# Kernel optimization log

Hardware: AMD Instinct MI355X
Metric: run time of the kernel (lower is better)

The kernel has to match this reference:

```python
import jax, jax.numpy as jnp
import numpy as np

B = 8388608
BASE_STABLE = 0.95
BASE_CHANGE = 0.05
TASK_WEIGHT = 1.0
EPS = 1e-8


def setup_inputs() -> dict:
    key = jax.random.key(0)
    k1, k2 = jax.random.split(key)
    logits = jax.random.normal(k1, (B, 2), dtype=jnp.float32)
    labels = jax.random.randint(k2, (B,), 0, 2, dtype=jnp.int64)
    return {"logits": logits, "labels": labels}


def reference(logits, labels):
    # softmax over class dim (C=2)
    p = jax.nn.softmax(logits, axis=1)
    p0 = p[:, 0]  # prob of 'stable' class
    p1 = p[:, 1]  # prob of 'change' class

    # Per-sample weights. In the original torch code these are computed via
    # .item() (python floats), i.e. they are constants w.r.t. autodiff.
    adj0 = jnp.maximum(0.0, p0 - BASE_STABLE) / (1.0 - BASE_STABLE)
    w0 = jnp.maximum(0.1, 1.0 - adj0 * 0.5)
    adj1 = jnp.maximum(0.0, p1 - BASE_CHANGE) / (1.0 - BASE_CHANGE)
    w1 = jnp.maximum(0.5, 2.0 - adj1)
    w0 = jax.lax.stop_gradient(w0)
    w1 = jax.lax.stop_gradient(w1)

    stable = labels == 0
    loss = jnp.where(stable,
                     -w0 * jnp.log(p0 + EPS),
                     -w1 * jnp.log(p1 + EPS))
    task_loss = loss.mean()
    total_loss = TASK_WEIGHT * task_loss
    return total_loss
```

## Files before the change

### kernel.cpp

```cpp
#include <hip/hip_runtime.h>


#define B_TOTAL   8388608
#define INV_B     (1.0f / 8388608.0f)
#define EPS_LOSS  1e-8f

#define NBLOCK    2048
#define NTHREAD   256
#define NTOT      (NBLOCK * NTHREAD)
#define NITER     (B_TOTAL / 2 / NTOT)

typedef float f4 __attribute__((ext_vector_type(4)));
typedef int   i2 __attribute__((ext_vector_type(2)));

__device__ __forceinline__ float row_loss(float l0, float l1, int label) {
    float d = l1 - l0;
    float x = __int_as_float(__float_as_int(d) ^ (label << 31));
    float e = __expf(x);
    float p = __builtin_amdgcn_rcpf(1.0f + e);
    bool chg   = (label != 0);
    float c    = chg ? 0.05f        : 0.95f;
    float b    = chg ? (1.0f/0.95f) : 10.0f;
    float a    = chg ? 2.0f         : 1.0f;
    float wmin = chg ? 0.5f         : 0.1f;
    float t = fmaxf(0.0f, p - c);
    float w = fmaxf(wmin, fmaf(-b, t, a));
    return -w * __logf(p + EPS_LOSS);
}

__global__ __launch_bounds__(NTHREAD, 8) void pal_loss_kernel(
        const f4* __restrict__ lg,
        const i2* __restrict__ lb,
        float* __restrict__ partials)
{
    int tid = blockIdx.x * NTHREAD + threadIdx.x;

    f4 L[NITER];
    i2 Y[NITER];
    #pragma unroll
    for (int k = 0; k < NITER; ++k) {
        L[k] = __builtin_nontemporal_load(lg + tid + k * NTOT);
        Y[k] = __builtin_nontemporal_load(lb + tid + k * NTOT);
    }
    __builtin_amdgcn_sched_barrier(0);

    float acc = 0.0f;
    #pragma unroll
    for (int k = 0; k < NITER; ++k) {
        acc += row_loss(L[k].x, L[k].y, Y[k].x);
        acc += row_loss(L[k].z, L[k].w, Y[k].y);
    }

    #pragma unroll
    for (int off = 32; off > 0; off >>= 1)
        acc += __shfl_down(acc, off, 64);

    __shared__ float wsum[NTHREAD / 64];
    int lane = threadIdx.x & 63;
    int wid  = threadIdx.x >> 6;
    if (lane == 0) wsum[wid] = acc;
    __syncthreads();

    if (threadIdx.x == 0)
        partials[blockIdx.x] = wsum[0] + wsum[1] + wsum[2] + wsum[3];
}

__global__ __launch_bounds__(NTHREAD) void pal_finalize_kernel(
        const float* __restrict__ partials,
        float* __restrict__ out)
{
    float acc = 0.0f;
    #pragma unroll
    for (int k = 0; k < NBLOCK / NTHREAD; ++k)
        acc += partials[threadIdx.x + k * NTHREAD];

    #pragma unroll
    for (int off = 32; off > 0; off >>= 1)
        acc += __shfl_down(acc, off, 64);

    __shared__ float wsum[NTHREAD / 64];
    int lane = threadIdx.x & 63;
    int wid  = threadIdx.x >> 6;
    if (lane == 0) wsum[wid] = acc;
    __syncthreads();

    if (threadIdx.x == 0)
        out[0] = (wsum[0] + wsum[1] + wsum[2] + wsum[3]) * INV_B;
}

extern "C" void kernel_launch(void* const* d_in, const int* in_sizes, int n_in,
                              void* d_out, int out_size, void* d_ws, size_t ws_size,
                              hipStream_t stream) {
    const f4* lg  = (const f4*)d_in[0];
    const i2* lb  = (const i2*)d_in[1];
    float*    out = (float*)d_out;
    float*    ws  = (float*)d_ws;

    pal_loss_kernel<<<NBLOCK, NTHREAD, 0, stream>>>(lg, lb, ws);
    pal_finalize_kernel<<<1, NTHREAD, 0, stream>>>(ws, out);
}
```

Before: 119.9 us.

## Double grid size and use 16-byte label loads with fewer rows per thread

Work is redistributed across twice as many blocks, each thread now handling 8 rows instead of 16. Labels are read as int4 vectors so every load is 16 bytes, and the logit loads are paired to match. Nontemporal loads and the occupancy hint in the launch bounds are dropped, and an empty asm statement replaces the sched_barrier to force all loads to issue before compute. The aim is more memory parallelism and wider transactions. The cost is more blocks, more partial sums for the finalize kernel, and the loss of the nontemporal cache hint.

Result: faster. 112.9 us (-5.8%).

```diff
diff --git a/kernel.cpp b/kernel.cpp
--- a/kernel.cpp
+++ b/kernel.cpp
@@ -5,13 +5,12 @@
 #define INV_B     (1.0f / 8388608.0f)
 #define EPS_LOSS  1e-8f
 
-#define NBLOCK    2048
+#define NBLOCK    4096
 #define NTHREAD   256
-#define NTOT      (NBLOCK * NTHREAD)
-#define NITER     (B_TOTAL / 2 / NTOT)
+#define NT        (NBLOCK * NTHREAD)
 
 typedef float f4 __attribute__((ext_vector_type(4)));
-typedef int   i2 __attribute__((ext_vector_type(2)));
+typedef int   i4 __attribute__((ext_vector_type(4)));
 
 __device__ __forceinline__ float row_loss(float l0, float l1, int label) {
     float d = l1 - l0;
@@ -28,28 +27,30 @@
     return -w * __logf(p + EPS_LOSS);
 }
 
-__global__ __launch_bounds__(NTHREAD, 8) void pal_loss_kernel(
+__global__ __launch_bounds__(NTHREAD) void pal_loss_kernel(
         const f4* __restrict__ lg,
-        const i2* __restrict__ lb,
+        const i4* __restrict__ lb,
         float* __restrict__ partials)
 {
-    int tid = blockIdx.x * NTHREAD + threadIdx.x;
+    int t = blockIdx.x * NTHREAD + threadIdx.x;
 
-    f4 L[NITER];
-    i2 Y[NITER];
-    #pragma unroll
-    for (int k = 0; k < NITER; ++k) {
-        L[k] = __builtin_nontemporal_load(lg + tid + k * NTOT);
-        Y[k] = __builtin_nontemporal_load(lb + tid + k * NTOT);
-    }
-    __builtin_amdgcn_sched_barrier(0);
+    i4 Y0  = lb[t];
+    i4 Y1  = lb[t + NT];
+    f4 L00 = lg[2 * t];
+    f4 L01 = lg[2 * t + 1];
+    f4 L10 = lg[2 * (t + NT)];
+    f4 L11 = lg[2 * (t + NT) + 1];
+    asm volatile("" :: "v"(Y0), "v"(Y1), "v"(L00), "v"(L01), "v"(L10), "v"(L11));
 
     float acc = 0.0f;
-    #pragma unroll
-    for (int k = 0; k < NITER; ++k) {
-        acc += row_loss(L[k].x, L[k].y, Y[k].x);
-        acc += row_loss(L[k].z, L[k].w, Y[k].y);
-    }
+    acc += row_loss(L00.x, L00.y, Y0.x);
+    acc += row_loss(L00.z, L00.w, Y0.y);
+    acc += row_loss(L01.x, L01.y, Y0.z);
+    acc += row_loss(L01.z, L01.w, Y0.w);
+    acc += row_loss(L10.x, L10.y, Y1.x);
+    acc += row_loss(L10.z, L10.w, Y1.y);
+    acc += row_loss(L11.x, L11.y, Y1.z);
+    acc += row_loss(L11.z, L11.w, Y1.w);
 
     #pragma unroll
     for (int off = 32; off > 0; off >>= 1)
@@ -92,7 +93,7 @@
                               void* d_out, int out_size, void* d_ws, size_t ws_size,
                               hipStream_t stream) {
     const f4* lg  = (const f4*)d_in[0];
-    const i2* lb  = (const i2*)d_in[1];
+    const i4* lb  = (const i4*)d_in[1];
     float*    out = (float*)d_out;
     float*    ws  = (float*)d_ws;
 
```
